# Performance work log

Hardware: AMD Instinct MI355X
Metric: run time of the kernel (lower is better)

Reference implementation:

```python
import jax, jax.numpy as jnp
import numpy as np

INPUT_SIZE, HIDDEN_SIZE, OUTPUT_SIZE = 2, 512, 512
ALPHA = 0.1


def setup_inputs() -> dict:
    key = jax.random.key(0)
    ks = jax.random.split(key, 8)
    B, T = 256, 512
    inputs = jax.random.normal(ks[0], (B, T, INPUT_SIZE), dtype=jnp.float32)
    init_context = jax.random.normal(ks[1], (B, OUTPUT_SIZE), dtype=jnp.float32)
    # parameters (torch Linear convention: y = x @ W.T + b)
    W_in = jax.random.normal(ks[2], (HIDDEN_SIZE, INPUT_SIZE), dtype=jnp.float32) * (1.0 / np.sqrt(INPUT_SIZE + HIDDEN_SIZE))
    b_in = jnp.zeros((HIDDEN_SIZE,), dtype=jnp.float32)
    # orthogonal-ish recurrent weight via QR
    A = jax.random.normal(ks[3], (HIDDEN_SIZE, HIDDEN_SIZE), dtype=jnp.float32)
    W_rec, _ = jnp.linalg.qr(A)
    W_rec = W_rec.astype(jnp.float32)
    b_rec = jnp.zeros((HIDDEN_SIZE,), dtype=jnp.float32)
    W_out = jax.random.normal(ks[4], (OUTPUT_SIZE, HIDDEN_SIZE), dtype=jnp.float32) * (1.0 / np.sqrt(HIDDEN_SIZE + OUTPUT_SIZE))
    W_h_init = jax.random.normal(ks[5], (HIDDEN_SIZE, OUTPUT_SIZE), dtype=jnp.float32) * (1.0 / np.sqrt(HIDDEN_SIZE + OUTPUT_SIZE))
    return {"inputs": inputs, "init_context": init_context, "W_in": W_in, "b_in": b_in,
            "W_rec": W_rec, "b_rec": b_rec, "W_out": W_out, "W_h_init": W_h_init}


def reference(inputs, init_context, W_in, b_in, W_rec, b_rec, W_out, W_h_init):
    # inputs: (B, T, I); init_context: (B, O)
    h0 = init_context @ W_h_init.T  # (B, H)
    # precompute input projection for all timesteps: (B, T, H)
    x_proj = jnp.einsum('bti,hi->bth', inputs, W_in) + b_in

    def step(h, x_t):
        h_new = (1.0 - ALPHA) * h + ALPHA * jnp.tanh(x_t + h @ W_rec.T + b_rec)
        return h_new, h_new

    # scan over time: move T to leading axis
    _, hs = jax.lax.scan(step, h0, jnp.swapaxes(x_proj, 0, 1))  # hs: (T, B, H)
    hidden_states = jnp.swapaxes(hs, 0, 1)  # (B, T, H)
    outputs = jnp.einsum('bth,oh->bto', hidden_states, W_out)  # (B, T, O)
    return hidden_states, outputs
```

## Files before the change

### kernel.cpp

```cpp
#include <hip/hip_runtime.h>

typedef __bf16 bf16x8 __attribute__((ext_vector_type(8)));
typedef float f32x4 __attribute__((ext_vector_type(4)));
typedef unsigned int u32x4 __attribute__((ext_vector_type(4)));

union UQ { uint4 q; u32x4 p; bf16x8 v; __bf16 b[8]; unsigned long long d[2]; };

__device__ __forceinline__ unsigned short f2bf(float x){
  union { float f; unsigned u; } c; c.f = x;
  return (unsigned short)((c.u + 0x7fffu + ((c.u >> 16) & 1u)) >> 16);
}

__global__ void pack_kernel(const float* __restrict__ W, uint4* __restrict__ dst){
  int tid  = blockIdx.x * 512 + threadIdx.x;
  int lane = tid & 63;
  int kt   = (tid >> 6) & 15;
  int ntl  = tid >> 10;
  int row  = ntl * 16 + (lane & 15);
  int k0   = kt * 32 + ((lane >> 4) << 3);
  const float* s = &W[row * 512 + k0];
  unsigned a0 = f2bf(s[0]) | ((unsigned)f2bf(s[1]) << 16);
  unsigned a1 = f2bf(s[2]) | ((unsigned)f2bf(s[3]) << 16);
  unsigned a2 = f2bf(s[4]) | ((unsigned)f2bf(s[5]) << 16);
  unsigned a3 = f2bf(s[6]) | ((unsigned)f2bf(s[7]) << 16);
  dst[tid] = (uint4){a0, a1, a2, a3};
}

__global__ void h0_kernel(const float* __restrict__ init, const float* __restrict__ Whi,
                          float* __restrict__ h0, unsigned short* __restrict__ hb0){
  int b = blockIdx.x, n = threadIdx.x;
  __shared__ float ic[512];
  ic[n] = init[b * 512 + n];
  __syncthreads();
  const float4* wr = (const float4*)&Whi[n * 512];
  float s = 0.f;
  #pragma unroll 8
  for (int o = 0; o < 128; o++){
    float4 w = wr[o];
    s += w.x * ic[4*o] + w.y * ic[4*o+1] + w.z * ic[4*o+2] + w.w * ic[4*o+3];
  }
  h0[b * 512 + n] = s;
  hb0[b * 512 + n] = f2bf(s);
}

__global__ __launch_bounds__(512, 2)
void rnn_kernel(const float* __restrict__ inputs, const float* __restrict__ W_in,
                const float* __restrict__ b_in, const float* __restrict__ b_rec,
                const uint4* __restrict__ wfrag, const float* __restrict__ h0,
                const unsigned short* __restrict__ hb0, float* __restrict__ hidden){
  const int m = blockIdx.x;
  const int g16 = m << 4;
  const int tid = threadIdx.x, w = tid >> 6, lane = tid & 63;
  const int col = lane & 15, quad = lane >> 4;
  const int nbase = w << 6;
  const int swc = (col & 7) << 3;

  __shared__ unsigned short hbuf[16 * 512];
  __shared__ uint4 wlds[8][16][64];

  UQ u[32];
  #pragma unroll
  for (int kt = 0; kt < 8; kt++)
    #pragma unroll
    for (int nt = 0; nt < 4; nt++){
      const uint4* src = &wfrag[(((w << 2) + nt) * 16 + kt) * 64 + lane];
      asm volatile("global_load_dwordx4 %0, %1, off"
                   : "=v"(u[kt * 4 + nt].p) : "v"(src) : "memory");
    }
  asm volatile("s_waitcnt vmcnt(0)" ::: "memory");
  #pragma unroll
  for (int j = 0; j < 32; j++)
    asm volatile("" : "+v"(u[j].d[0]), "+v"(u[j].d[1]));

  #pragma unroll
  for (int kt = 8; kt < 12; kt++)
    #pragma unroll
    for (int nt = 0; nt < 4; nt++)
      wlds[w][(kt - 8) * 4 + nt][lane] = wfrag[(((w << 2) + nt) * 16 + kt) * 64 + lane];

  UQ uaug[4];
  #pragma unroll
  for (int nt = 0; nt < 4; nt++){
    uaug[nt].d[0] = 0; uaug[nt].d[1] = 0;
    if (quad == 0){
      int n = nbase + nt * 16 + col;
      uaug[nt].b[0] = (__bf16)W_in[2 * n];
      uaug[nt].b[1] = (__bf16)W_in[2 * n + 1];
      uaug[nt].b[2] = (__bf16)(b_in[n] + b_rec[n]);
    }
  }

  float h[16];
  #pragma unroll
  for (int nt = 0; nt < 4; nt++){
    float4 h4 = *(const float4*)&h0[(g16 + col) * 512 + nbase + nt * 16 + (quad << 2)];
    h[nt*4+0] = h4.x; h[nt*4+1] = h4.y; h[nt*4+2] = h4.z; h[nt*4+3] = h4.w;
  }

  {
    int b = tid >> 5, n0 = (tid & 31) << 4;
    const uint4* s4 = (const uint4*)&hb0[(g16 + b) * 512 + n0];
    uint4 v0 = s4[0], v1 = s4[1];
    int sw = (b & 7) << 3;
    *(uint4*)&hbuf[(b << 9) + (n0 ^ sw)]       = v0;
    *(uint4*)&hbuf[(b << 9) + ((n0 + 8) ^ sw)] = v1;
  }
  __syncthreads();

  unsigned long long wsp = (unsigned long long)wfrag;
  const float2* xsrc = (const float2*)&inputs[((size_t)(g16 + col)) << 10];

#define ISSUE(b4) { int kt_ = 12 + (b4);                                          \
    _Pragma("unroll")                                                             \
    for (int nt_ = 0; nt_ < 4; nt_++)                                             \
      sv[(b4)*4 + nt_].q = ws[(((w << 2) + nt_) * 16 + kt_) * 64 + lane]; }

  for (int t = 0; t < 512; t++){
    asm volatile("" : "+s"(wsp));
    const uint4* ws = (const uint4*)wsp;

    UQ baug; baug.d[0] = 0; baug.d[1] = 0;
    float2 xv = xsrc[t];
    if (quad == 0){
      baug.b[0] = (__bf16)xv.x; baug.b[1] = (__bf16)xv.y; baug.b[2] = (__bf16)1.0f;
    }

    f32x4 acc[4];
    #pragma unroll
    for (int nt = 0; nt < 4; nt++)
      acc[nt] = __builtin_amdgcn_mfma_f32_16x16x32_bf16(uaug[nt].v, baug.v,
                                                        (f32x4){0.f,0.f,0.f,0.f}, 0, 0, 0);

    UQ sv[16];
    ISSUE(0);
    #pragma unroll
    for (int kt = 0; kt < 8; kt++){
      UQ bfr;
      bfr.q = *(const uint4*)&hbuf[(col << 9) + (((kt << 5) + (quad << 3)) ^ swc)];
      #pragma unroll
      for (int nt = 0; nt < 4; nt++)
        acc[nt] = __builtin_amdgcn_mfma_f32_16x16x32_bf16(u[kt*4+nt].v, bfr.v, acc[nt], 0, 0, 0);
      if (kt == 0) ISSUE(1);
      if (kt == 2) ISSUE(2);
      if (kt == 4) ISSUE(3);
    }
    #pragma unroll
    for (int kt = 8; kt < 12; kt++){
      UQ bfr;
      bfr.q = *(const uint4*)&hbuf[(col << 9) + (((kt << 5) + (quad << 3)) ^ swc)];
      #pragma unroll
      for (int nt = 0; nt < 4; nt++){
        UQ a; a.q = wlds[w][(kt - 8) * 4 + nt][lane];
        acc[nt] = __builtin_amdgcn_mfma_f32_16x16x32_bf16(a.v, bfr.v, acc[nt], 0, 0, 0);
      }
    }
    #pragma unroll
    for (int kt = 12; kt < 16; kt++){
      UQ bfr;
      bfr.q = *(const uint4*)&hbuf[(col << 9) + (((kt << 5) + (quad << 3)) ^ swc)];
      #pragma unroll
      for (int nt = 0; nt < 4; nt++)
        acc[nt] = __builtin_amdgcn_mfma_f32_16x16x32_bf16(sv[(kt-12)*4+nt].v, bfr.v, acc[nt], 0, 0, 0);
    }

    __syncthreads();

    #pragma unroll
    for (int nt = 0; nt < 4; nt++){
      UQ hw; hw.d[0] = 0; hw.d[1] = 0;
      #pragma unroll
      for (int r = 0; r < 4; r++){
        float z  = acc[nt][r];
        float e  = __expf(2.0f * z);
        float rc = __builtin_amdgcn_rcpf(e + 1.0f);
        float hn = fmaf(0.9f, h[nt*4+r], 0.1f) - 0.2f * rc;
        h[nt*4+r] = hn;
        hw.b[r] = (__bf16)hn;
      }
      *(unsigned long long*)&hbuf[(col << 9) + ((nbase + (nt << 4) + (quad << 2)) ^ swc)] = hw.d[0];
      *(float4*)&hidden[((size_t)(g16 + col) * 512 + t) * 512 + nbase + (nt << 4) + (quad << 2)] =
          (float4){h[nt*4+0], h[nt*4+1], h[nt*4+2], h[nt*4+3]};
    }
    __syncthreads();
  }
#undef ISSUE
}

__global__ __launch_bounds__(512, 2)
void out_gemm(const float* __restrict__ hidden, const uint4* __restrict__ wofrag,
              float* __restrict__ outp){
  const int tid  = threadIdx.x;
  const int w    = tid >> 6;
  const int lane = tid & 63;
  const int col  = lane & 15;
  const int quad = lane >> 4;
  const int ms   = w >> 1;
  const int nh   = w & 1;
  const int m0   = blockIdx.x << 7;

  __shared__ unsigned short albf[128 * 32];

  f32x4 acc[2][16];
  #pragma unroll
  for (int mt = 0; mt < 2; mt++)
    #pragma unroll
    for (int nt = 0; nt < 16; nt++) acc[mt][nt] = (f32x4){0.f, 0.f, 0.f, 0.f};

  for (int kt = 0; kt < 16; kt++){
    #pragma unroll
    for (int i = 0; i < 2; i++){
      int r  = (tid >> 3) + (i << 6);
      int c4 = (tid & 7) << 2;
      float4 v = *(const float4*)&hidden[(m0 + r) * 512 + (kt << 5) + c4];
      unsigned lo = f2bf(v.x) | ((unsigned)f2bf(v.y) << 16);
      unsigned hi = f2bf(v.z) | ((unsigned)f2bf(v.w) << 16);
      int byteoff = (r << 6) + ((c4 << 1) ^ (((r >> 1) & 3) << 4));
      *(uint2*)((char*)albf + byteoff) = (uint2){lo, hi};
    }
    __syncthreads();

    bf16x8 af[2];
    #pragma unroll
    for (int mt = 0; mt < 2; mt++){
      int rl = (ms << 5) + (mt << 4) + col;
      int byteoff = (rl << 6) + ((quad << 4) ^ (((rl >> 1) & 3) << 4));
      af[mt] = *(const bf16x8*)((const char*)albf + byteoff);
    }

    #pragma unroll
    for (int nt = 0; nt < 16; nt++){
      UQ u; u.q = wofrag[((((nh << 4) + nt) << 4) + kt) * 64 + lane];
      acc[0][nt] = __builtin_amdgcn_mfma_f32_16x16x32_bf16(af[0], u.v, acc[0][nt], 0, 0, 0);
      acc[1][nt] = __builtin_amdgcn_mfma_f32_16x16x32_bf16(af[1], u.v, acc[1][nt], 0, 0, 0);
    }
    __syncthreads();
  }

  #pragma unroll
  for (int mt = 0; mt < 2; mt++)
    #pragma unroll
    for (int nt = 0; nt < 16; nt++)
      #pragma unroll
      for (int r = 0; r < 4; r++)
        outp[(m0 + (ms << 5) + (mt << 4) + (quad << 2) + r) * 512
             + (nh << 8) + (nt << 4) + col] = acc[mt][nt][r];
}

extern "C" void kernel_launch(void* const* d_in, const int* in_sizes, int n_in,
                              void* d_out, int out_size, void* d_ws, size_t ws_size,
                              hipStream_t stream){
  const float* inputs  = (const float*)d_in[0];
  const float* initc   = (const float*)d_in[1];
  const float* W_in    = (const float*)d_in[2];
  const float* b_in    = (const float*)d_in[3];
  const float* W_rec   = (const float*)d_in[4];
  const float* b_rec   = (const float*)d_in[5];
  const float* W_out   = (const float*)d_in[6];
  const float* W_hi    = (const float*)d_in[7];

  float* hidden  = (float*)d_out;
  float* outputs = hidden + (size_t)67108864;

  char* ws = (char*)d_ws;
  uint4*          wrec_f = (uint4*)ws;
  uint4*          wout_f = (uint4*)(ws + (512 << 10));
  float*          h0     = (float*)(ws + (1024 << 10));
  unsigned short* hb0    = (unsigned short*)(ws + (1536 << 10));

  pack_kernel<<<64, 512, 0, stream>>>(W_rec, wrec_f);
  pack_kernel<<<64, 512, 0, stream>>>(W_out, wout_f);
  h0_kernel<<<256, 512, 0, stream>>>(initc, W_hi, h0, hb0);
  rnn_kernel<<<16, 512, 0, stream>>>(inputs, W_in, b_in, b_rec, wrec_f, h0, hb0, hidden);
  out_gemm<<<1024, 512, 0, stream>>>(hidden, wout_f, outputs);
}
```

Baseline: 1.719 ms.

## Rebalance recurrent weight tiers, stagger LDS reads, and stage whole A tile in out_gemm

Result: slower. 2.528 ms (+47.1%).

```diff
diff --git a/kernel.cpp b/kernel.cpp
--- a/kernel.cpp
+++ b/kernel.cpp
@@ -43,7 +43,7 @@
   hb0[b * 512 + n] = f2bf(s);
 }
 
-__global__ __launch_bounds__(512, 2)
+__global__ __launch_bounds__(512, 1)
 void rnn_kernel(const float* __restrict__ inputs, const float* __restrict__ W_in,
                 const float* __restrict__ b_in, const float* __restrict__ b_rec,
                 const uint4* __restrict__ wfrag, const float* __restrict__ h0,
@@ -56,7 +56,7 @@
   const int swc = (col & 7) << 3;
 
   __shared__ unsigned short hbuf[16 * 512];
-  __shared__ uint4 wlds[8][16][64];
+  __shared__ uint4 wlds[8][8][64];
 
   UQ u[32];
   #pragma unroll
@@ -73,7 +73,7 @@
     asm volatile("" : "+v"(u[j].d[0]), "+v"(u[j].d[1]));
 
   #pragma unroll
-  for (int kt = 8; kt < 12; kt++)
+  for (int kt = 8; kt < 10; kt++)
     #pragma unroll
     for (int nt = 0; nt < 4; nt++)
       wlds[w][(kt - 8) * 4 + nt][lane] = wfrag[(((w << 2) + nt) * 16 + kt) * 64 + lane];
@@ -109,11 +109,39 @@
 
   unsigned long long wsp = (unsigned long long)wfrag;
   const float2* xsrc = (const float2*)&inputs[((size_t)(g16 + col)) << 10];
-
-#define ISSUE(b4) { int kt_ = 12 + (b4);                                          \
+  const bool ldsw_first = (w & 1);
+
+#define ISSUE(b2) {                    \
     _Pragma("unroll")                                                             \
-    for (int nt_ = 0; nt_ < 4; nt_++)                                             \
-      sv[(b4)*4 + nt_].q = ws[(((w << 2) + nt_) * 16 + kt_) * 64 + lane]; }
+    for (int kk_ = 0; kk_ < 2; kk_++){                                            \
+      const int kt_ = 10 + 2*(b2) + kk_;                                          \
+      _Pragma("unroll")                                                           \
+      for (int nt_ = 0; nt_ < 4; nt_++)                                           \
+        sv[(kt_-10)*4 + nt_].q = ws[(((w << 2) + nt_) * 16 + kt_) * 64 + lane];   \
+    } }
+
+#define HREAD(kt_) *(const uint4*)&hbuf[(col << 9) + ((((kt_) << 5) + (quad << 3)) ^ swc)]
+
+#define TIER_REG {                                                                \
+    _Pragma("unroll")                                                             \
+    for (int kt = 0; kt < 8; kt++){                                               \
+      UQ bfr; bfr.q = HREAD(kt);                                                  \
+      _Pragma("unroll")                                                           \
+      for (int nt = 0; nt < 4; nt++)                                              \
+        acc[nt] = __builtin_amdgcn_mfma_f32_16x16x32_bf16(u[kt*4+nt].v, bfr.v, acc[nt], 0, 0, 0); \
+      if (kt == 2) ISSUE(1);                                                      \
+      if (kt == 5) ISSUE(2);                                                      \
+    } }
+
+#define TIER_LDSW {                                                               \
+    _Pragma("unroll")                                                             \
+    for (int kt = 8; kt < 10; kt++){                                              \
+      UQ bfr; bfr.q = HREAD(kt);                                                  \
+      _Pragma("unroll")                                                           \
+      for (int nt = 0; nt < 4; nt++){                                             \
+        UQ a; a.q = wlds[w][(kt - 8) * 4 + nt][lane];                             \
+        acc[nt] = __builtin_amdgcn_mfma_f32_16x16x32_bf16(a.v, bfr.v, acc[nt], 0, 0, 0); \
+      } } }
 
   for (int t = 0; t < 512; t++){
     asm volatile("" : "+s"(wsp));
@@ -131,37 +159,19 @@
       acc[nt] = __builtin_amdgcn_mfma_f32_16x16x32_bf16(uaug[nt].v, baug.v,
                                                         (f32x4){0.f,0.f,0.f,0.f}, 0, 0, 0);
 
-    UQ sv[16];
+    UQ sv[24];
     ISSUE(0);
-    #pragma unroll
-    for (int kt = 0; kt < 8; kt++){
-      UQ bfr;
-      bfr.q = *(const uint4*)&hbuf[(col << 9) + (((kt << 5) + (quad << 3)) ^ swc)];
+    __builtin_amdgcn_s_setprio(1);
+    if (ldsw_first){ TIER_LDSW; TIER_REG; }
+    else           { TIER_REG; TIER_LDSW; }
+    #pragma unroll
+    for (int kt = 10; kt < 16; kt++){
+      UQ bfr; bfr.q = HREAD(kt);
       #pragma unroll
       for (int nt = 0; nt < 4; nt++)
-        acc[nt] = __builtin_amdgcn_mfma_f32_16x16x32_bf16(u[kt*4+nt].v, bfr.v, acc[nt], 0, 0, 0);
-      if (kt == 0) ISSUE(1);
-      if (kt == 2) ISSUE(2);
-      if (kt == 4) ISSUE(3);
-    }
-    #pragma unroll
-    for (int kt = 8; kt < 12; kt++){
-      UQ bfr;
-      bfr.q = *(const uint4*)&hbuf[(col << 9) + (((kt << 5) + (quad << 3)) ^ swc)];
-      #pragma unroll
-      for (int nt = 0; nt < 4; nt++){
-        UQ a; a.q = wlds[w][(kt - 8) * 4 + nt][lane];
-        acc[nt] = __builtin_amdgcn_mfma_f32_16x16x32_bf16(a.v, bfr.v, acc[nt], 0, 0, 0);
-      }
-    }
-    #pragma unroll
-    for (int kt = 12; kt < 16; kt++){
-      UQ bfr;
-      bfr.q = *(const uint4*)&hbuf[(col << 9) + (((kt << 5) + (quad << 3)) ^ swc)];
-      #pragma unroll
-      for (int nt = 0; nt < 4; nt++)
-        acc[nt] = __builtin_amdgcn_mfma_f32_16x16x32_bf16(sv[(kt-12)*4+nt].v, bfr.v, acc[nt], 0, 0, 0);
-    }
+        acc[nt] = __builtin_amdgcn_mfma_f32_16x16x32_bf16(sv[(kt-10)*4+nt].v, bfr.v, acc[nt], 0, 0, 0);
+    }
+    __builtin_amdgcn_s_setprio(0);
 
     __syncthreads();
 
@@ -184,9 +194,12 @@
     __syncthreads();
   }
 #undef ISSUE
-}
-
-__global__ __launch_bounds__(512, 2)
+#undef HREAD
+#undef TIER_REG
+#undef TIER_LDSW
+}
+
+__global__ __launch_bounds__(512, 1)
 void out_gemm(const float* __restrict__ hidden, const uint4* __restrict__ wofrag,
               float* __restrict__ outp){
   const int tid  = threadIdx.x;
@@ -198,7 +211,20 @@
   const int nh   = w & 1;
   const int m0   = blockIdx.x << 7;
 
-  __shared__ unsigned short albf[128 * 32];
+  __shared__ unsigned short albf[128 * 512];
+
+  #pragma unroll 4
+  for (int i = 0; i < 32; i++){
+    int idx = i * 512 + tid;
+    int r   = idx >> 7;
+    int c4  = (idx & 127) << 2;
+    float4 v = *(const float4*)&hidden[(size_t)(m0 + r) * 512 + c4];
+    unsigned lo = f2bf(v.x) | ((unsigned)f2bf(v.y) << 16);
+    unsigned hi = f2bf(v.z) | ((unsigned)f2bf(v.w) << 16);
+    int byteoff = (r << 10) + (((c4 << 1)) ^ ((r & 7) << 4));
+    *(uint2*)((char*)albf + byteoff) = (uint2){lo, hi};
+  }
+  __syncthreads();
 
   f32x4 acc[2][16];
   #pragma unroll
@@ -207,33 +233,19 @@
     for (int nt = 0; nt < 16; nt++) acc[mt][nt] = (f32x4){0.f, 0.f, 0.f, 0.f};
 
   for (int kt = 0; kt < 16; kt++){
-    #pragma unroll
-    for (int i = 0; i < 2; i++){
-      int r  = (tid >> 3) + (i << 6);
-      int c4 = (tid & 7) << 2;
-      float4 v = *(const float4*)&hidden[(m0 + r) * 512 + (kt << 5) + c4];
-      unsigned lo = f2bf(v.x) | ((unsigned)f2bf(v.y) << 16);
-      unsigned hi = f2bf(v.z) | ((unsigned)f2bf(v.w) << 16);
-      int byteoff = (r << 6) + ((c4 << 1) ^ (((r >> 1) & 3) << 4));
-      *(uint2*)((char*)albf + byteoff) = (uint2){lo, hi};
-    }
-    __syncthreads();
-
     bf16x8 af[2];
     #pragma unroll
     for (int mt = 0; mt < 2; mt++){
       int rl = (ms << 5) + (mt << 4) + col;
-      int byteoff = (rl << 6) + ((quad << 4) ^ (((rl >> 1) & 3) << 4));
+      int byteoff = (rl << 10) + (((kt << 6) + (quad << 4)) ^ ((rl & 7) << 4));
       af[mt] = *(const bf16x8*)((const char*)albf + byteoff);
     }
-
     #pragma unroll
     for (int nt = 0; nt < 16; nt++){
       UQ u; u.q = wofrag[((((nh << 4) + nt) << 4) + kt) * 64 + lane];
       acc[0][nt] = __builtin_amdgcn_mfma_f32_16x16x32_bf16(af[0], u.v, acc[0][nt], 0, 0, 0);
       acc[1][nt] = __builtin_amdgcn_mfma_f32_16x16x32_bf16(af[1], u.v, acc[1][nt], 0, 0, 0);
     }
-    __syncthreads();
   }
 
   #pragma unroll
@@ -242,7 +254,7 @@
     for (int nt = 0; nt < 16; nt++)
       #pragma unroll
       for (int r = 0; r < 4; r++)
-        outp[(m0 + (ms << 5) + (mt << 4) + (quad << 2) + r) * 512
+        outp[(size_t)(m0 + (ms << 5) + (mt << 4) + (quad << 2) + r) * 512
              + (nh << 8) + (nt << 4) + col] = acc[mt][nt][r];
 }
 
```
